# Performance work log

Measured on AMD Instinct MI355X. Metric: run time of the kernel, lower is better.

The kernel has to match this reference:

```python
import jax, jax.numpy as jnp
import numpy as np

B = 4_000_000

# physical constants from initBatteryParams
R_ = 8.3144621
F_ = 96487.0
ALPHA = 0.5
SN = 0.0002
SP = 0.0002
KN = 20000.0
KP = 20000.0
VOL = 2.2e-05
VOLS = 0.1 * VOL
VOLB = VOL - VOLS
TO = 10.0
TSN = 90.0
TSP = 90.0
U0P = 4.03
U0N = 0.01
QMAX_BASE = 10000.0
RO_BASE = 10.0
T_DIFFUSION = 7.0e6  # repo default; attribute used in getNextState
DT = 1.0


def setup_inputs() -> dict:
    key = jax.random.key(0)
    ks = jax.random.split(key, 12)
    qMax = 1.4 * jnp.ones((B,), jnp.float32)   # 14000/qMaxBASE
    Ro = 0.015 * jnp.ones((B,), jnp.float32)   # 0.15/RoBASE
    # physically plausible initial state (get_initial_state) + small noise
    qM = qMax * QMAX_BASE  # [B]
    Tb = 292.1 + 0.5 * jax.random.normal(ks[0], (B, 1), jnp.float32)
    Vo = 0.01 * jax.random.uniform(ks[1], (B, 1), jnp.float32)
    Vsn = 0.01 * jax.random.uniform(ks[2], (B, 1), jnp.float32)
    Vsp = 0.01 * jax.random.uniform(ks[3], (B, 1), jnp.float32)
    jitter = lambda k: 1.0 + 0.01 * jax.random.normal(k, (B, 1), jnp.float32)
    qnB = (qM * 0.6 * VOLB / VOL)[:, None] * jitter(ks[4])
    qnS = (qM * 0.6 * VOLS / VOL)[:, None] * jitter(ks[5])
    qpB = (qM * 0.4 * VOLB / VOL)[:, None] * jitter(ks[6])
    qpS = (qM * 0.4 * VOLS / VOL)[:, None] * jitter(ks[7])
    states = jnp.concatenate([Tb, Vo, Vsn, Vsp, qnB, qnS, qpB, qpS], axis=1)
    inputs = 1.0 + 2.0 * jax.random.uniform(ks[8], (B, 1), jnp.float32)  # current [A]
    kw = jax.random.split(ks[9], 8)
    return {
        "inputs": inputs, "states": states, "qMax": qMax, "Ro": Ro,
        "Wp0": 0.5 * jax.random.normal(kw[0], (8, 1), jnp.float32),
        "bp0": 0.1 * jax.random.normal(kw[1], (8,), jnp.float32),
        "Wp2": 0.5 * jax.random.normal(kw[2], (4, 8), jnp.float32),
        "bp2": 0.1 * jax.random.normal(kw[3], (4,), jnp.float32),
        "Wp4": 0.5 * jax.random.normal(kw[4], (1, 4), jnp.float32),
        "bp4": 0.1 * jax.random.normal(kw[5], (1,), jnp.float32),
        "Wn": 0.0016 * jnp.ones((1, 1), jnp.float32),  # ~fitted Linear(1,1)
        "bn": -0.0008 * jnp.ones((1,), jnp.float32),
    }


def _mlp_p(x, Wp0, bp0, Wp2, bp2, Wp4, bp4):
    h = jnp.tanh(x @ Wp0.T + bp0)
    h = jnp.tanh(h @ Wp2.T + bp2)
    return h @ Wp4.T + bp4


def _cell(inputs, states, qMax, Ro, Wp0, bp0, Wp2, bp2, Wp4, bp4, Wn, bn):
    Tb, Vo, Vsn, Vsp, qnB, qnS, qpB, qpS = jnp.split(states, 8, axis=1)
    i = inputs  # [B,1]
    qSMax = (qMax * QMAX_BASE * VOLS / VOL)[:, None]  # [B,1]
    # --- getNextState ---
    xpS = jnp.clip(qpS / qSMax, 1e-18, 1.0)
    xnS = jnp.clip(qnS / qSMax, 1e-18, 1.0)
    Jn0 = 1e-18 + KN * (1.0 - xnS) ** ALPHA * xnS ** ALPHA
    Jp0 = 1e-18 + KP * (1.0 - xpS) ** ALPHA * xpS ** ALPHA
    qdotDiffusionBSn = (qnB / VOLB - qnS / VOLS) / T_DIFFUSION
    qdotDiffusionBSp = (qpB / VOLB - qpS / VOLS) / T_DIFFUSION
    Jn = i / SN
    Jp = i / SP
    VoNominal = i * Ro[:, None] * RO_BASE
    VsnNominal = R_ * Tb / F_ / ALPHA * jnp.arcsinh(Jn / (2.0 * Jn0))
    VspNominal = R_ * Tb / F_ / ALPHA * jnp.arcsinh(Jp / (2.0 * Jp0))
    Tb2 = Tb  # Tbdot = 0
    Vo2 = Vo + (VoNominal - Vo) / TO * DT
    Vsn2 = Vsn + (VsnNominal - Vsn) / TSN * DT
    Vsp2 = Vsp + (VspNominal - Vsp) / TSP * DT
    qnB2 = qnB + (-qdotDiffusionBSn) * DT
    qnS2 = qnS + (qdotDiffusionBSn - i) * DT
    qpB2 = qpB + (-qdotDiffusionBSp) * DT
    qpS2 = qpS + (i + qdotDiffusionBSp) * DT
    XNew = jnp.concatenate([Tb2, Vo2, Vsn2, Vsp2, qnB2, qnS2, qpB2, qpS2], axis=1)
    # --- getNextOutput (on XNew) ---
    xpS_o = qpS2 / qSMax
    xnS_o = qnS2 / qSMax
    VepMLP = _mlp_p(xpS_o, Wp0, bp0, Wp2, bp2, Wp4, bp4)
    VenMLP = xnS_o @ Wn.T + bn
    safe_log_p = jnp.clip((1.0 - xpS_o) / xpS_o, 1e-18, 1e18)
    safe_log_n = jnp.clip((1.0 - xnS_o) / xnS_o, 1e-18, 1e18)
    Vep = U0P + R_ * Tb2 / F_ * jnp.log(safe_log_p) + VepMLP
    Ven = U0N + R_ * Tb2 / F_ * jnp.log(safe_log_n) + VenMLP
    V = Vep - Ven - Vo2 - Vsn2 - Vsp2
    return V, XNew


def reference(inputs, states, qMax, Ro, Wp0, bp0, Wp2, bp2, Wp4, bp4, Wn, bn):
    return _cell(inputs, states, qMax, Ro, Wp0, bp0, Wp2, bp2, Wp4, bp4, Wn, bn)
```

## Files before the change

### kernel.cpp

```cpp
#include <hip/hip_runtime.h>
#include <math.h>

typedef float v4f __attribute__((ext_vector_type(4)));
typedef float v2f __attribute__((ext_vector_type(2)));

#define RTF       (8.3144621f / 96487.0f)
#define VOLS_     2.2e-06f
#define VOLB_     1.98e-05f
#define INV_TDIFF (1.0f / 7.0e6f)

#define LUT_N 2048
#define BLOCK 512

__device__ __forceinline__ float asinh_pos(float x) {
    return __logf(x + sqrtf(fmaf(x, x, 1.0f)));
}

__device__ __forceinline__ float jval(float x) {
    float j0 = 1e-18f + 20000.0f * sqrtf(fmaxf(x * (1.0f - x), 0.0f));
    return 1.0f / (2.0f * j0);
}

__device__ __forceinline__ void mlp_log_eval(
    float x,
    const float* __restrict__ Wp0, const float* __restrict__ bp0,
    const float* __restrict__ Wp2, const float* __restrict__ bp2,
    const float* __restrict__ Wp4, const float* __restrict__ bp4,
    float* mlp_out, float* log_out)
{
    float h1[8];
#pragma unroll
    for (int j = 0; j < 8; j++)
        h1[j] = tanhf(fmaf(x, Wp0[j], bp0[j]));
    float mlp = bp4[0];
#pragma unroll
    for (int k = 0; k < 4; k++) {
        float a = bp2[k];
#pragma unroll
        for (int j = 0; j < 8; j++)
            a = fmaf(h1[j], Wp2[k * 8 + j], a);
        mlp = fmaf(tanhf(a), Wp4[k], mlp);
    }
    *mlp_out = mlp;
    float r = fminf(fmaxf((1.0f - x) / fmaxf(x, 1e-30f), 1e-18f), 1e18f);
    *log_out = RTF * logf(r);
}

__global__ __launch_bounds__(256) void build_lut_kernel(
    const float* __restrict__ Wp0, const float* __restrict__ bp0,
    const float* __restrict__ Wp2, const float* __restrict__ bp2,
    const float* __restrict__ Wp4, const float* __restrict__ bp4,
    v2f* __restrict__ lutJ2, v4f* __restrict__ lutO4)
{
    int idx = blockIdx.x * blockDim.x + threadIdx.x;
    if (idx >= LUT_N) return;
    const float dx = 1.0f / (float)(LUT_N - 1);
    float x0 = (float)idx * dx;
    float x1 = fminf(x0 + dx, 1.0f);

    v2f j; j.x = jval(x0); j.y = jval(x1);
    lutJ2[idx] = j;

    float m0, l0, m1, l1;
    mlp_log_eval(x0, Wp0, bp0, Wp2, bp2, Wp4, bp4, &m0, &l0);
    mlp_log_eval(x1, Wp0, bp0, Wp2, bp2, Wp4, bp4, &m1, &l1);
    v4f o; o.x = m0; o.y = l0; o.z = m1; o.w = l1;
    lutO4[idx] = o;
}

__global__ __launch_bounds__(BLOCK) void battery_cell_kernel(
    const float* __restrict__ inp,
    const float* __restrict__ st,
    const float* __restrict__ qMaxp,
    const float* __restrict__ Rop,
    const float* __restrict__ Wn,
    const float* __restrict__ bn,
    const float* __restrict__ lutG,
    float* __restrict__ outV,
    float* __restrict__ outX,
    int B)
{
    __shared__ float slut[12288];

    int b = blockIdx.x * BLOCK + threadIdx.x;

    bool active = (b < B);
    int bc = active ? b : 0;
    const v4f* st4 = (const v4f*)st;
    v4f s0 = st4[2 * bc];
    v4f s1 = st4[2 * bc + 1];
    float i  = inp[bc];
    float qm = qMaxp[bc];
    float ro = Rop[bc];
    float wn = Wn[0], wbn = bn[0];

    {
        const v4f* src = (const v4f*)lutG;
        v4f* dst = (v4f*)slut;
#pragma unroll
        for (int k = 0; k < 6; k++)
            dst[threadIdx.x + k * BLOCK] = src[threadIdx.x + k * BLOCK];
    }
    __syncthreads();
    const v2f* lutJ2 = (const v2f*)slut;
    const v4f* lutO4 = (const v4f*)(slut + 4096);

    if (!active) return;

    float Tb  = s0.x, Vo  = s0.y, Vsn = s0.z, Vsp = s0.w;
    float qnB = s1.x, qnS = s1.y, qpB = s1.z, qpS = s1.w;

    float invq = __fdividef(1.0f, qm * 1000.0f);

    float xpS = fminf(fmaxf(qpS * invq, 1e-18f), 1.0f);
    float xnS = fminf(fmaxf(qnS * invq, 1e-18f), 1.0f);

    float tn = xnS * (float)(LUT_N - 1);
    float tp = xpS * (float)(LUT_N - 1);
    int in0 = min((int)tn, LUT_N - 2);
    int ip0 = min((int)tp, LUT_N - 2);
    float fn = tn - (float)in0;
    float fp = tp - (float)ip0;
    v2f jn = lutJ2[in0];
    v2f jp = lutJ2[ip0];
    float inv2Jn = fmaf(fn, jn.y - jn.x, jn.x);
    float inv2Jp = fmaf(fp, jp.y - jp.x, jp.x);

    float qdotn = (qnB * (1.0f / VOLB_) - qnS * (1.0f / VOLS_)) * INV_TDIFF;
    float qdotp = (qpB * (1.0f / VOLB_) - qpS * (1.0f / VOLS_)) * INV_TDIFF;

    float Jn     = i * 5000.0f;
    float VoNom  = i * ro * 10.0f;
    float coef   = RTF * Tb * 2.0f;
    float VsnNom = coef * asinh_pos(Jn * inv2Jn);
    float VspNom = coef * asinh_pos(Jn * inv2Jp);

    float Vo2  = Vo  + (VoNom  - Vo ) * 0.1f;
    float Vsn2 = Vsn + (VsnNom - Vsn) * (1.0f / 90.0f);
    float Vsp2 = Vsp + (VspNom - Vsp) * (1.0f / 90.0f);
    float qnB2 = qnB - qdotn;
    float qnS2 = qnS + qdotn - i;
    float qpB2 = qpB - qdotp;
    float qpS2 = qpS + i + qdotp;

    float xp = qpS2 * invq;
    float xn = qnS2 * invq;

    float tpo = fminf(fmaxf(xp, 0.0f), 1.0f) * (float)(LUT_N - 1);
    float tno = fminf(fmaxf(xn, 0.0f), 1.0f) * (float)(LUT_N - 1);
    int ipo = min((int)tpo, LUT_N - 2);
    int ino = min((int)tno, LUT_N - 2);
    float fpo = tpo - (float)ipo;
    float fno = tno - (float)ino;
    v4f op = lutO4[ipo];
    v4f on = lutO4[ino];
    float mlp_p = fmaf(fpo, op.z - op.x, op.x);
    float log_p = fmaf(fpo, op.w - op.y, op.y);
    float log_n = fmaf(fno, on.w - on.y, on.y);

    float Vep = 4.03f + Tb * log_p + mlp_p;
    float Ven = 0.01f + Tb * log_n + fmaf(xn, wn, wbn);
    float V = Vep - Ven - Vo2 - Vsn2 - Vsp2;

    outV[b] = V;
    v4f o0; o0.x = Tb;   o0.y = Vo2;  o0.z = Vsn2; o0.w = Vsp2;
    v4f o1; o1.x = qnB2; o1.y = qnS2; o1.z = qpB2; o1.w = qpS2;
    v4f* ox4 = (v4f*)outX;
    ox4[2 * b]     = o0;
    ox4[2 * b + 1] = o1;
}

extern "C" void kernel_launch(void* const* d_in, const int* in_sizes, int n_in,
                              void* d_out, int out_size, void* d_ws, size_t ws_size,
                              hipStream_t stream) {
    const float* inp  = (const float*)d_in[0];
    const float* st   = (const float*)d_in[1];
    const float* qMax = (const float*)d_in[2];
    const float* Ro   = (const float*)d_in[3];
    const float* Wp0  = (const float*)d_in[4];
    const float* bp0  = (const float*)d_in[5];
    const float* Wp2  = (const float*)d_in[6];
    const float* bp2  = (const float*)d_in[7];
    const float* Wp4  = (const float*)d_in[8];
    const float* bp4  = (const float*)d_in[9];
    const float* Wn   = (const float*)d_in[10];
    const float* bn   = (const float*)d_in[11];

    int B = in_sizes[0];
    float* outV = (float*)d_out;
    float* outX = (float*)d_out + B;

    v2f* lutJ2 = (v2f*)d_ws;
    v4f* lutO4 = (v4f*)((char*)d_ws + LUT_N * 8);

    build_lut_kernel<<<LUT_N / 256, 256, 0, stream>>>(
        Wp0, bp0, Wp2, bp2, Wp4, bp4, lutJ2, lutO4);

    int grid = (B + BLOCK - 1) / BLOCK;
    battery_cell_kernel<<<grid, BLOCK, 0, stream>>>(
        inp, st, qMax, Ro, Wn, bn, (const float*)d_ws, outV, outX, B);
}
```

Before: 292.0 us.

## Read LUT from global memory in a grid-stride loop instead of LDS staging

The per-block copy of the lookup table into shared memory and its barrier are removed. Threads now gather LUT entries directly from global memory, relying on the cache, inside a persistent grid-stride loop with a fixed grid of 2048 blocks of 256 threads. The LUT resolution doubles to 4096 entries, which improves interpolation accuracy but gives a larger cache footprint. The aim is to stop every block from refetching 48KB of table and to cut the LDS pressure that limited occupancy, at the cost of scattered L1/L2 gathers.

```diff
diff --git a/kernel.cpp b/kernel.cpp
--- a/kernel.cpp
+++ b/kernel.cpp
@@ -9,8 +9,9 @@
 #define VOLB_     1.98e-05f
 #define INV_TDIFF (1.0f / 7.0e6f)
 
-#define LUT_N 2048
-#define BLOCK 512
+#define LUT_N 4096
+#define BLOCK 256
+#define GRID  2048
 
 __device__ __forceinline__ float asinh_pos(float x) {
     return __logf(x + sqrtf(fmaf(x, x, 1.0f)));
@@ -75,99 +76,85 @@
     const float* __restrict__ Rop,
     const float* __restrict__ Wn,
     const float* __restrict__ bn,
-    const float* __restrict__ lutG,
+    const v2f*   __restrict__ lutJ2,
+    const v4f*   __restrict__ lutO4,
     float* __restrict__ outV,
     float* __restrict__ outX,
     int B)
 {
-    __shared__ float slut[12288];
-
-    int b = blockIdx.x * BLOCK + threadIdx.x;
-
-    bool active = (b < B);
-    int bc = active ? b : 0;
     const v4f* st4 = (const v4f*)st;
-    v4f s0 = st4[2 * bc];
-    v4f s1 = st4[2 * bc + 1];
-    float i  = inp[bc];
-    float qm = qMaxp[bc];
-    float ro = Rop[bc];
+    v4f* ox4 = (v4f*)outX;
     float wn = Wn[0], wbn = bn[0];
 
-    {
-        const v4f* src = (const v4f*)lutG;
-        v4f* dst = (v4f*)slut;
-#pragma unroll
-        for (int k = 0; k < 6; k++)
-            dst[threadIdx.x + k * BLOCK] = src[threadIdx.x + k * BLOCK];
+    int stride = GRID * BLOCK;
+    for (int b = blockIdx.x * BLOCK + threadIdx.x; b < B; b += stride) {
+        v4f s0 = st4[2 * b];
+        v4f s1 = st4[2 * b + 1];
+        float i  = inp[b];
+        float qm = qMaxp[b];
+        float ro = Rop[b];
+
+        float Tb  = s0.x, Vo  = s0.y, Vsn = s0.z, Vsp = s0.w;
+        float qnB = s1.x, qnS = s1.y, qpB = s1.z, qpS = s1.w;
+
+        float invq = __fdividef(1.0f, qm * 1000.0f);
+
+        float xpS = fminf(fmaxf(qpS * invq, 1e-18f), 1.0f);
+        float xnS = fminf(fmaxf(qnS * invq, 1e-18f), 1.0f);
+
+        float tn = xnS * (float)(LUT_N - 1);
+        float tp = xpS * (float)(LUT_N - 1);
+        int in0 = min((int)tn, LUT_N - 2);
+        int ip0 = min((int)tp, LUT_N - 2);
+        float fn = tn - (float)in0;
+        float fp = tp - (float)ip0;
+        v2f jn = lutJ2[in0];
+        v2f jp = lutJ2[ip0];
+        float inv2Jn = fmaf(fn, jn.y - jn.x, jn.x);
+        float inv2Jp = fmaf(fp, jp.y - jp.x, jp.x);
+
+        float qdotn = (qnB * (1.0f / VOLB_) - qnS * (1.0f / VOLS_)) * INV_TDIFF;
+        float qdotp = (qpB * (1.0f / VOLB_) - qpS * (1.0f / VOLS_)) * INV_TDIFF;
+
+        float Jn     = i * 5000.0f;
+        float VoNom  = i * ro * 10.0f;
+        float coef   = RTF * Tb * 2.0f;
+        float VsnNom = coef * asinh_pos(Jn * inv2Jn);
+        float VspNom = coef * asinh_pos(Jn * inv2Jp);
+
+        float Vo2  = Vo  + (VoNom  - Vo ) * 0.1f;
+        float Vsn2 = Vsn + (VsnNom - Vsn) * (1.0f / 90.0f);
+        float Vsp2 = Vsp + (VspNom - Vsp) * (1.0f / 90.0f);
+        float qnB2 = qnB - qdotn;
+        float qnS2 = qnS + qdotn - i;
+        float qpB2 = qpB - qdotp;
+        float qpS2 = qpS + i + qdotp;
+
+        float xp = qpS2 * invq;
+        float xn = qnS2 * invq;
+
+        float tpo = fminf(fmaxf(xp, 0.0f), 1.0f) * (float)(LUT_N - 1);
+        float tno = fminf(fmaxf(xn, 0.0f), 1.0f) * (float)(LUT_N - 1);
+        int ipo = min((int)tpo, LUT_N - 2);
+        int ino = min((int)tno, LUT_N - 2);
+        float fpo = tpo - (float)ipo;
+        float fno = tno - (float)ino;
+        v4f op = lutO4[ipo];
+        v4f on = lutO4[ino];
+        float mlp_p = fmaf(fpo, op.z - op.x, op.x);
+        float log_p = fmaf(fpo, op.w - op.y, op.y);
+        float log_n = fmaf(fno, on.w - on.y, on.y);
+
+        float Vep = 4.03f + Tb * log_p + mlp_p;
+        float Ven = 0.01f + Tb * log_n + fmaf(xn, wn, wbn);
+        float V = Vep - Ven - Vo2 - Vsn2 - Vsp2;
+
+        outV[b] = V;
+        v4f o0; o0.x = Tb;   o0.y = Vo2;  o0.z = Vsn2; o0.w = Vsp2;
+        v4f o1; o1.x = qnB2; o1.y = qnS2; o1.z = qpB2; o1.w = qpS2;
+        ox4[2 * b]     = o0;
+        ox4[2 * b + 1] = o1;
     }
-    __syncthreads();
-    const v2f* lutJ2 = (const v2f*)slut;
-    const v4f* lutO4 = (const v4f*)(slut + 4096);
-
-    if (!active) return;
-
-    float Tb  = s0.x, Vo  = s0.y, Vsn = s0.z, Vsp = s0.w;
-    float qnB = s1.x, qnS = s1.y, qpB = s1.z, qpS = s1.w;
-
-    float invq = __fdividef(1.0f, qm * 1000.0f);
-
-    float xpS = fminf(fmaxf(qpS * invq, 1e-18f), 1.0f);
-    float xnS = fminf(fmaxf(qnS * invq, 1e-18f), 1.0f);
-
-    float tn = xnS * (float)(LUT_N - 1);
-    float tp = xpS * (float)(LUT_N - 1);
-    int in0 = min((int)tn, LUT_N - 2);
-    int ip0 = min((int)tp, LUT_N - 2);
-    float fn = tn - (float)in0;
-    float fp = tp - (float)ip0;
-    v2f jn = lutJ2[in0];
-    v2f jp = lutJ2[ip0];
-    float inv2Jn = fmaf(fn, jn.y - jn.x, jn.x);
-    float inv2Jp = fmaf(fp, jp.y - jp.x, jp.x);
-
-    float qdotn = (qnB * (1.0f / VOLB_) - qnS * (1.0f / VOLS_)) * INV_TDIFF;
-    float qdotp = (qpB * (1.0f / VOLB_) - qpS * (1.0f / VOLS_)) * INV_TDIFF;
-
-    float Jn     = i * 5000.0f;
-    float VoNom  = i * ro * 10.0f;
-    float coef   = RTF * Tb * 2.0f;
-    float VsnNom = coef * asinh_pos(Jn * inv2Jn);
-    float VspNom = coef * asinh_pos(Jn * inv2Jp);
-
-    float Vo2  = Vo  + (VoNom  - Vo ) * 0.1f;
-    float Vsn2 = Vsn + (VsnNom - Vsn) * (1.0f / 90.0f);
-    float Vsp2 = Vsp + (VspNom - Vsp) * (1.0f / 90.0f);
-    float qnB2 = qnB - qdotn;
-    float qnS2 = qnS + qdotn - i;
-    float qpB2 = qpB - qdotp;
-    float qpS2 = qpS + i + qdotp;
-
-    float xp = qpS2 * invq;
-    float xn = qnS2 * invq;
-
-    float tpo = fminf(fmaxf(xp, 0.0f), 1.0f) * (float)(LUT_N - 1);
-    float tno = fminf(fmaxf(xn, 0.0f), 1.0f) * (float)(LUT_N - 1);
-    int ipo = min((int)tpo, LUT_N - 2);
-    int ino = min((int)tno, LUT_N - 2);
-    float fpo = tpo - (float)ipo;
-    float fno = tno - (float)ino;
-    v4f op = lutO4[ipo];
-    v4f on = lutO4[ino];
-    float mlp_p = fmaf(fpo, op.z - op.x, op.x);
-    float log_p = fmaf(fpo, op.w - op.y, op.y);
-    float log_n = fmaf(fno, on.w - on.y, on.y);
-
-    float Vep = 4.03f + Tb * log_p + mlp_p;
-    float Ven = 0.01f + Tb * log_n + fmaf(xn, wn, wbn);
-    float V = Vep - Ven - Vo2 - Vsn2 - Vsp2;
-
-    outV[b] = V;
-    v4f o0; o0.x = Tb;   o0.y = Vo2;  o0.z = Vsn2; o0.w = Vsp2;
-    v4f o1; o1.x = qnB2; o1.y = qnS2; o1.z = qpB2; o1.w = qpS2;
-    v4f* ox4 = (v4f*)outX;
-    ox4[2 * b]     = o0;
-    ox4[2 * b + 1] = o1;
 }
 
 extern "C" void kernel_launch(void* const* d_in, const int* in_sizes, int n_in,
@@ -196,7 +183,6 @@
     build_lut_kernel<<<LUT_N / 256, 256, 0, stream>>>(
         Wp0, bp0, Wp2, bp2, Wp4, bp4, lutJ2, lutO4);
 
-    int grid = (B + BLOCK - 1) / BLOCK;
-    battery_cell_kernel<<<grid, BLOCK, 0, stream>>>(
-        inp, st, qMax, Ro, Wn, bn, (const float*)d_ws, outV, outX, B);
+    battery_cell_kernel<<<GRID, BLOCK, 0, stream>>>(
+        inp, st, qMax, Ro, Wn, bn, lutJ2, lutO4, outV, outX, B);
 }
```

Result: slower. 308.0 us (+5.5%).
